# Kernel tuning notes

Hardware: AMD Instinct MI355X
Metric: run time of the kernel (lower is better)

Reference implementation:

```python
import jax, jax.numpy as jnp
import numpy as np

NUM_RHS_EMB = 100000
NUM_TYPES = 64
NUM_LHS_EMB = 100000
NUM_RHS_IDXS = 8192
NUM_LHS_IDXS = 8192


def setup_inputs() -> dict:
    key = jax.random.key(0)
    k1, k2, k3, k4, k5 = jax.random.split(key, 5)
    return {
        # tf.random_normal_initializer default stddev = 0.05
        "rhs_type_scores": jax.random.normal(k1, (NUM_RHS_EMB, NUM_TYPES), jnp.float32) * 0.05,
        "type_lhs_scores": jax.random.normal(k2, (NUM_TYPES, NUM_LHS_EMB), jnp.float32) * 0.05,
        "lhs_nonterminal_bias": jax.random.normal(k3, (1, NUM_LHS_EMB), jnp.float32),
        "rhs_emb_idxs": jax.random.randint(k4, (NUM_RHS_IDXS,), 0, NUM_RHS_EMB, dtype=jnp.int32),
        "lhs_emb_idxs": jax.random.randint(k5, (NUM_LHS_IDXS,), 0, NUM_LHS_EMB, dtype=jnp.int32),
    }


def _log_matmul_exp(a, b):
    # Numerically stable log(exp(a) @ exp(b)): a [L, M], b [M, N] -> [L, N]
    max_a = jnp.max(a, axis=1, keepdims=True)  # [L, 1]
    max_b = jnp.max(b, axis=0, keepdims=True)  # [1, N]
    c = jnp.log(jnp.exp(a - max_a) @ jnp.exp(b - max_b))
    return c + max_a + max_b


def reference(rhs_type_scores, type_lhs_scores, lhs_nonterminal_bias, rhs_emb_idxs, lhs_emb_idxs):
    temperature = 1.0
    # gather rows of rhs scores for the batch: [R, K]
    rts = jnp.take(rhs_type_scores, rhs_emb_idxs, axis=0)
    logp_type_given_rhs = jax.nn.log_softmax(rts / temperature, axis=1)  # [R, K]
    # softmax over the FULL lhs vocab (approximate_denominator=False)
    logp_lhs_given_type = jax.nn.log_softmax(
        type_lhs_scores / temperature + lhs_nonterminal_bias, axis=1
    )  # [K, num_lhs_emb]
    logp_lhs_given_type = jnp.take(logp_lhs_given_type, lhs_emb_idxs, axis=1)  # [K, L]
    logp_lhs_given_rhs = _log_matmul_exp(logp_type_given_rhs, logp_lhs_given_type)  # [R, L]
    return logp_lhs_given_rhs.T  # [L, R]
```

## Files before the change

kernel.cpp:

```cpp
#include <hip/hip_runtime.h>
#include <hip/hip_bf16.h>

#define NUM_RHS_EMB 100000
#define NUM_TYPES   64
#define NUM_LHS_EMB 100000
#define NR 8192
#define NL 8192
#define LSE_CHUNKS 25
#define LSE_CHUNK  4000
#define LSE_BLOCKS (NUM_TYPES * LSE_CHUNKS)
#define ASIDE_BLOCKS (NR / 4)

typedef __attribute__((ext_vector_type(8))) short short8;
typedef __attribute__((ext_vector_type(4))) float f32x4;

__device__ __forceinline__ ushort f2b(float x) {
    unsigned u = __builtin_bit_cast(unsigned, x);
    unsigned r = u + 0x7fffu + ((u >> 16) & 1u);
    return (ushort)(r >> 16);
}

__global__ __launch_bounds__(256) void prep1_kernel(
    const float* __restrict__ t, const float* __restrict__ bias, float2* __restrict__ part,
    const float* __restrict__ rts, const int* __restrict__ ridx,
    ushort* __restrict__ ea, float* __restrict__ ma) {
    const int tid = threadIdx.x;
    if (blockIdx.x < LSE_BLOCKS) {
        const int k = blockIdx.x / LSE_CHUNKS;
        const int c = blockIdx.x % LSE_CHUNKS;
        const float4* __restrict__ row = (const float4*)(t + (size_t)k * NUM_LHS_EMB + c * LSE_CHUNK);
        const float4* __restrict__ bb  = (const float4*)(bias + c * LSE_CHUNK);
        __shared__ float red[4];
        const int w = tid >> 6;

        float m = -1e30f;
        for (int j = tid; j < LSE_CHUNK / 4; j += 256) {
            float4 tv = row[j], bv = bb[j];
            m = fmaxf(m, fmaxf(fmaxf(tv.x + bv.x, tv.y + bv.y), fmaxf(tv.z + bv.z, tv.w + bv.w)));
        }
        #pragma unroll
        for (int d = 1; d < 64; d <<= 1) m = fmaxf(m, __shfl_xor(m, d));
        if ((tid & 63) == 0) red[w] = m;
        __syncthreads();
        m = fmaxf(fmaxf(red[0], red[1]), fmaxf(red[2], red[3]));
        __syncthreads();

        float s = 0.f;
        for (int j = tid; j < LSE_CHUNK / 4; j += 256) {
            float4 tv = row[j], bv = bb[j];
            s += expf(tv.x + bv.x - m) + expf(tv.y + bv.y - m)
               + expf(tv.z + bv.z - m) + expf(tv.w + bv.w - m);
        }
        #pragma unroll
        for (int d = 1; d < 64; d <<= 1) s += __shfl_xor(s, d);
        if ((tid & 63) == 0) red[w] = s;
        __syncthreads();
        if (tid == 0) part[blockIdx.x] = make_float2(m, red[0] + red[1] + red[2] + red[3]);
    } else {
        const int r = (blockIdx.x - LSE_BLOCKS) * 4 + (tid >> 6);
        const int k = tid & 63;
        const float v = rts[(size_t)ridx[r] * 64 + k];
        float m = v;
        #pragma unroll
        for (int d = 1; d < 64; d <<= 1) m = fmaxf(m, __shfl_xor(m, d));
        const float e = expf(v - m);
        float s = e;
        #pragma unroll
        for (int d = 1; d < 64; d <<= 1) s += __shfl_xor(s, d);
        ea[(size_t)r * 64 + k] = f2b(e);
        if (k == 0) ma[r] = -logf(s);
    }
}

__global__ __launch_bounds__(256) void bside_kernel(
    const float* __restrict__ t, const float* __restrict__ bias,
    const int* __restrict__ lidx, const float2* __restrict__ part,
    ushort* __restrict__ ebt, float* __restrict__ mb) {
    __shared__ float lse_s[NUM_TYPES];
    const int tid = threadIdx.x;
    if (tid < NUM_TYPES) {
        float2 p[LSE_CHUNKS];
        #pragma unroll
        for (int c = 0; c < LSE_CHUNKS; c++) p[c] = part[tid * LSE_CHUNKS + c];
        float M = -1e30f;
        #pragma unroll
        for (int c = 0; c < LSE_CHUNKS; c++) M = fmaxf(M, p[c].x);
        float S = 0.f;
        #pragma unroll
        for (int c = 0; c < LSE_CHUNKS; c++) S += p[c].y * expf(p[c].x - M);
        lse_s[tid] = M + logf(S);
    }
    __syncthreads();

    const int l = blockIdx.x * 4 + (tid >> 6);
    const int k = tid & 63;
    const int j = lidx[l];
    const float v = t[(size_t)k * NUM_LHS_EMB + j] - lse_s[k];
    float m = v;
    #pragma unroll
    for (int d = 1; d < 64; d <<= 1) m = fmaxf(m, __shfl_xor(m, d));
    ebt[(size_t)l * 64 + k] = f2b(expf(v - m));
    if (k == 0) mb[l] = m + bias[j];
}

__global__ __launch_bounds__(256) void gemm_kernel(
    const ushort* __restrict__ B_ea,
    const ushort* __restrict__ A_ebt,
    const float* __restrict__ ma, const float* __restrict__ mb,
    float* __restrict__ out) {
    const int bm = blockIdx.x & 63;
    const int bn = blockIdx.x >> 6;
    const int w = threadIdx.x >> 6, lane = threadIdx.x & 63;
    const int Moff = bm * 128 + (w >> 1) * 64;
    const int Noff = bn * 128 + (w & 1) * 64;
    const int lrow = lane & 15;
    const int lk = (lane >> 4) * 8;
    const int rq = (lane >> 4) * 4;

    f32x4 acc[4][4] = {};
    #pragma unroll
    for (int kb = 0; kb < 64; kb += 32) {
        short8 a[4], b[4];
        #pragma unroll
        for (int i = 0; i < 4; i++)
            a[i] = *(const short8*)(B_ea + (size_t)(Noff + i * 16 + lrow) * 64 + kb + lk);
        #pragma unroll
        for (int j = 0; j < 4; j++)
            b[j] = *(const short8*)(A_ebt + (size_t)(Moff + j * 16 + lrow) * 64 + kb + lk);
        #pragma unroll
        for (int i = 0; i < 4; i++)
            #pragma unroll
            for (int j = 0; j < 4; j++)
                acc[i][j] = __builtin_amdgcn_mfma_f32_16x16x32_bf16(a[i], b[j], acc[i][j], 0, 0, 0);
    }

    f32x4 mav[4];
    #pragma unroll
    for (int i = 0; i < 4; i++) mav[i] = *(const f32x4*)(ma + Noff + i * 16 + rq);

    #pragma unroll
    for (int j = 0; j < 4; j++) {
        const int l_out = Moff + j * 16 + lrow;
        const float mbv = mb[l_out];
        float* __restrict__ orow = out + (size_t)l_out * NR + Noff;
        #pragma unroll
        for (int i = 0; i < 4; i++) {
            f32x4 v;
            #pragma unroll
            for (int jr = 0; jr < 4; jr++)
                v[jr] = __logf(acc[i][j][jr]) + mav[i][jr] + mbv;
            *(f32x4*)(orow + i * 16 + rq) = v;
        }
    }
}

extern "C" void kernel_launch(void* const* d_in, const int* in_sizes, int n_in,
                              void* d_out, int out_size, void* d_ws, size_t ws_size,
                              hipStream_t stream) {
    const float* rts  = (const float*)d_in[0];
    const float* tls  = (const float*)d_in[1];
    const float* bias = (const float*)d_in[2];
    const int* ridx   = (const int*)d_in[3];
    const int* lidx   = (const int*)d_in[4];
    float* out = (float*)d_out;

    char* ws = (char*)d_ws;
    ushort* ea   = (ushort*)ws;
    ushort* ebt  = (ushort*)(ws + (size_t)NR * 64 * 2);
    float* ma    = (float*)(ws + (size_t)(NR + NL) * 64 * 2);
    float* mb    = (float*)(ws + (size_t)(NR + NL) * 64 * 2 + NR * 4);
    float2* part = (float2*)(ws + (size_t)(NR + NL) * 64 * 2 + (NR + NL) * 4);

    prep1_kernel<<<LSE_BLOCKS + ASIDE_BLOCKS, 256, 0, stream>>>(tls, bias, part, rts, ridx, ea, ma);
    bside_kernel<<<NL / 4, 256, 0, stream>>>(tls, bias, lidx, part, ebt, mb);
    gemm_kernel<<<(NL / 128) * (NR / 128), 256, 0, stream>>>(ea, ebt, ma, mb, out);
}
```

Before: 84.97 us.

## Retile output GEMM to 32x1024 blocks with wide per-wave N strips

Changes the GEMM block tile from 128x128 to 32 rows of L by 1024 columns of R, with each wave covering a 32x256 strip. The aim is long contiguous output row writes for the 256 MB fp32 output, which is the dominant cost, and more B-side reuse per wave. In exchange each wave reloads ea rows with less reuse across L, and the per-wave tile shape changes register use and the MFMA-to-load ratio.

```diff
diff --git a/kernel.cpp b/kernel.cpp
--- a/kernel.cpp
+++ b/kernel.cpp
@@ -10,6 +10,11 @@
 #define LSE_CHUNK  4000
 #define LSE_BLOCKS (NUM_TYPES * LSE_CHUNKS)
 #define ASIDE_BLOCKS (NR / 4)
+
+#define BM 32
+#define BN 1024
+#define NBN (NR / BN)
+#define NBM (NL / BM)
 
 typedef __attribute__((ext_vector_type(8))) short short8;
 typedef __attribute__((ext_vector_type(4))) float f32x4;
@@ -104,51 +109,44 @@
 }
 
 __global__ __launch_bounds__(256) void gemm_kernel(
-    const ushort* __restrict__ B_ea,
-    const ushort* __restrict__ A_ebt,
+    const ushort* __restrict__ ea,
+    const ushort* __restrict__ ebt,
     const float* __restrict__ ma, const float* __restrict__ mb,
     float* __restrict__ out) {
-    const int bm = blockIdx.x & 63;
-    const int bn = blockIdx.x >> 6;
+    const int bn = blockIdx.x & (NBN - 1);
+    const int bm = blockIdx.x >> 3;
     const int w = threadIdx.x >> 6, lane = threadIdx.x & 63;
-    const int Moff = bm * 128 + (w >> 1) * 64;
-    const int Noff = bn * 128 + (w & 1) * 64;
+    const int Moff = bm * BM;
+    const int Noff = bn * BN + w * 256;
     const int lrow = lane & 15;
     const int lk = (lane >> 4) * 8;
     const int rq = (lane >> 4) * 4;
 
-    f32x4 acc[4][4] = {};
+    f32x4 acc[16][2] = {};
     #pragma unroll
     for (int kb = 0; kb < 64; kb += 32) {
-        short8 a[4], b[4];
+        const short8 b0 = *(const short8*)(ebt + (size_t)(Moff + lrow) * 64 + kb + lk);
+        const short8 b1 = *(const short8*)(ebt + (size_t)(Moff + 16 + lrow) * 64 + kb + lk);
         #pragma unroll
-        for (int i = 0; i < 4; i++)
-            a[i] = *(const short8*)(B_ea + (size_t)(Noff + i * 16 + lrow) * 64 + kb + lk);
-        #pragma unroll
-        for (int j = 0; j < 4; j++)
-            b[j] = *(const short8*)(A_ebt + (size_t)(Moff + j * 16 + lrow) * 64 + kb + lk);
-        #pragma unroll
-        for (int i = 0; i < 4; i++)
-            #pragma unroll
-            for (int j = 0; j < 4; j++)
-                acc[i][j] = __builtin_amdgcn_mfma_f32_16x16x32_bf16(a[i], b[j], acc[i][j], 0, 0, 0);
+        for (int i = 0; i < 16; i++) {
+            const short8 a = *(const short8*)(ea + (size_t)(Noff + i * 16 + lrow) * 64 + kb + lk);
+            acc[i][0] = __builtin_amdgcn_mfma_f32_16x16x32_bf16(a, b0, acc[i][0], 0, 0, 0);
+            acc[i][1] = __builtin_amdgcn_mfma_f32_16x16x32_bf16(a, b1, acc[i][1], 0, 0, 0);
+        }
     }
 
-    f32x4 mav[4];
     #pragma unroll
-    for (int i = 0; i < 4; i++) mav[i] = *(const f32x4*)(ma + Noff + i * 16 + rq);
-
-    #pragma unroll
-    for (int j = 0; j < 4; j++) {
+    for (int j = 0; j < 2; j++) {
         const int l_out = Moff + j * 16 + lrow;
         const float mbv = mb[l_out];
         float* __restrict__ orow = out + (size_t)l_out * NR + Noff;
         #pragma unroll
-        for (int i = 0; i < 4; i++) {
+        for (int i = 0; i < 16; i++) {
+            const f32x4 mv = *(const f32x4*)(ma + Noff + i * 16 + rq);
             f32x4 v;
             #pragma unroll
             for (int jr = 0; jr < 4; jr++)
-                v[jr] = __logf(acc[i][j][jr]) + mav[i][jr] + mbv;
+                v[jr] = __logf(acc[i][j][jr]) + mv[jr] + mbv;
             *(f32x4*)(orow + i * 16 + rq) = v;
         }
     }
@@ -173,5 +171,5 @@
 
     prep1_kernel<<<LSE_BLOCKS + ASIDE_BLOCKS, 256, 0, stream>>>(tls, bias, part, rts, ridx, ea, ma);
     bside_kernel<<<NL / 4, 256, 0, stream>>>(tls, bias, lidx, part, ebt, mb);
-    gemm_kernel<<<(NL / 128) * (NR / 128), 256, 0, stream>>>(ea, ebt, ma, mb, out);
+    gemm_kernel<<<NBM * NBN, 256, 0, stream>>>(ea, ebt, ma, mb, out);
 }
```

Result: slower. 106.2 us (+25.0%).
